# Performance work log

Measured on AMD Instinct MI355X. Metric: run time of the kernel, lower is better.

The kernel has to match this reference:

```python
import jax, jax.numpy as jnp
import numpy as np
import math

D_MODEL = 512
N_HEADS = 8
K_NEIGHBORS = 30
B, S = 4, 2048
N_VARIATES = 8
EPS = 1e-5


def layer_norm(x, g, b):
    m = jnp.mean(x, axis=-1, keepdims=True)
    v = jnp.mean(jnp.square(x - m), axis=-1, keepdims=True)
    return (x - m) * jax.lax.rsqrt(v + EPS) * g + b


def mha(x, mask, w_in, b_in, w_out, b_out):
    # x: [B,S,D]; mask: [B,S,S] bool, True = blocked (same for every head)
    Bb, Ss, D = x.shape
    H, dh = N_HEADS, D // N_HEADS
    qkv = x @ w_in.T + b_in                      # [B,S,3D]
    q, k, v = jnp.split(qkv, 3, axis=-1)
    q = q.reshape(Bb, Ss, H, dh).transpose(0, 2, 1, 3)
    k = k.reshape(Bb, Ss, H, dh).transpose(0, 2, 1, 3)
    v = v.reshape(Bb, Ss, H, dh).transpose(0, 2, 1, 3)
    scores = jnp.einsum('bhqd,bhkd->bhqk', q, k) / math.sqrt(dh)
    scores = jnp.where(mask[:, None, :, :], -jnp.inf, scores)
    attn = jax.nn.softmax(scores, axis=-1)
    o = jnp.einsum('bhqk,bhkd->bhqd', attn, v)
    o = o.transpose(0, 2, 1, 3).reshape(Bb, Ss, D)
    return o @ w_out.T + b_out


def build_masks(variates, times, valid_mask):
    Bb, Ss = variates.shape
    eye = jnp.eye(Ss, dtype=bool)
    same_var = variates[:, :, None] == variates[:, None, :]      # [B,S,S]
    valid_2d = valid_mask[:, :, None] & valid_mask[:, None, :]
    intra_mask = ~(same_var & valid_2d)                          # True = blocked
    blocked_i = jnp.any(jnp.all(intra_mask, axis=-1))
    intra_mask = intra_mask & ~(blocked_i & eye)                 # unblock diagonal if any row fully blocked

    diff_var = ~same_var
    time_dist = jnp.abs(times[:, :, None] - times[:, None, :])
    time_dist = jnp.where(~valid_2d | ~diff_var, jnp.inf, time_dist)
    k = min(K_NEIGHBORS, Ss)
    _, topk_idx = jax.lax.top_k(-time_dist, k)                   # k smallest distances
    b_idx = jnp.arange(Bb)[:, None, None]
    r_idx = jnp.arange(Ss)[None, :, None]
    knn_mask = jnp.zeros((Bb, Ss, Ss), dtype=bool).at[b_idx, r_idx, topk_idx].set(True)
    knn_mask = knn_mask & valid_2d
    inter_mask = ~knn_mask
    blocked_e = jnp.any(jnp.all(inter_mask, axis=-1))
    inter_mask = inter_mask & ~(blocked_e & eye)
    return intra_mask, inter_mask


def setup_inputs() -> dict:
    key = jax.random.key(0)
    ks = jax.random.split(key, 12)
    D = D_MODEL
    s = 0.02
    inp = {
        'x': jax.random.normal(ks[0], (B, S, D), dtype=jnp.float32),
        'variates': jax.random.randint(ks[1], (B, S), 0, N_VARIATES),
        'times': jax.random.uniform(ks[2], (B, S), dtype=jnp.float32),
        'valid_mask': jnp.ones((B, S), dtype=bool),
        'in_w1': jax.random.normal(ks[3], (3 * D, D), dtype=jnp.float32) * s,
        'in_b1': jnp.zeros((3 * D,), dtype=jnp.float32),
        'out_w1': jax.random.normal(ks[4], (D, D), dtype=jnp.float32) * s,
        'out_b1': jnp.zeros((D,), dtype=jnp.float32),
        'ln_g1': jnp.ones((D,), dtype=jnp.float32),
        'ln_b1': jnp.zeros((D,), dtype=jnp.float32),
        'in_w2': jax.random.normal(ks[5], (3 * D, D), dtype=jnp.float32) * s,
        'in_b2': jnp.zeros((3 * D,), dtype=jnp.float32),
        'out_w2': jax.random.normal(ks[6], (D, D), dtype=jnp.float32) * s,
        'out_b2': jnp.zeros((D,), dtype=jnp.float32),
        'ln_g2': jnp.ones((D,), dtype=jnp.float32),
        'ln_b2': jnp.zeros((D,), dtype=jnp.float32),
    }
    return inp


def reference(x, variates, times, valid_mask,
              in_w1, in_b1, out_w1, out_b1, ln_g1, ln_b1,
              in_w2, in_b2, out_w2, out_b2, ln_g2, ln_b2):
    intra_mask, inter_mask = build_masks(variates, times, valid_mask)
    a1 = mha(x, intra_mask, in_w1, in_b1, out_w1, out_b1)
    x = layer_norm(x + a1, ln_g1, ln_b1)
    a2 = mha(x, inter_mask, in_w2, in_b2, out_w2, out_b2)
    x = layer_norm(x + a2, ln_g2, ln_b2)
    return x
```

## Files before the change

### kernel.cpp

```cpp
#include <hip/hip_runtime.h>


#define S_LEN 2048
#define BATCH 4
#define DM    512
#define NH    8
#define DH    64
#define KNN_K 30
#define NVAR  8
#define NTOK  (BATCH * S_LEN)
#define QKVD  (3 * DM)
#define PADCAP 2560
#define MAXTILE 40

typedef float f32x4 __attribute__((ext_vector_type(4)));
typedef short s16x8 __attribute__((ext_vector_type(8)));
typedef short s16x4 __attribute__((ext_vector_type(4)));

__device__ __forceinline__ float bf2f(short u) {
  return __uint_as_float(((unsigned)(unsigned short)u) << 16);
}
__device__ __forceinline__ short f2bf(float f) {
  unsigned x = __float_as_uint(f);
  return (short)((x + 0x7fffu + ((x >> 16) & 1u)) >> 16);
}

#define KNNB (NTOK / 8)
#define C_N0 (NTOK * DM / 4)
#define C_N1 (QKVD * DM / 4)
#define C_N2 (DM * DM / 4)
#define C_B1 (C_N0 + C_N1)
#define C_B2 (C_B1 + C_N2)
#define C_B3 (C_B2 + C_N1)
#define C_B4 (C_B3 + C_N2)
#define PREP_GRID (KNNB + BATCH + C_B4 / 256)

__global__ __launch_bounds__(256) void prep_all(
    const int* __restrict__ variates, const float* __restrict__ times,
    int* __restrict__ knn_out,
    int* __restrict__ gcnt, int* __restrict__ pgoff, int* __restrict__ porig,
    int* __restrict__ tileV, int* __restrict__ tileQ0, int* __restrict__ ntile,
    const float* __restrict__ s0, const float* __restrict__ s1,
    const float* __restrict__ s2, const float* __restrict__ s3,
    const float* __restrict__ s4, short* __restrict__ d0,
    short* __restrict__ d1, short* __restrict__ d2,
    short* __restrict__ d3, short* __restrict__ d4) {
  int blk = blockIdx.x;
  int tid = threadIdx.x;

  if (blk < KNNB) {
    int w = tid >> 6, lane = tid & 63;
    int bq0 = blk * 8 + w * 2;
    int bq1 = bq0 + 1;
    int b = bq0 >> 11;
    float tq0 = times[bq0], tq1 = times[bq1];
    int vq0 = variates[bq0], vq1 = variates[bq1];
    const float* tb = times + b * S_LEN;
    const int* vb = variates + b * S_LEN;
    int j0 = lane * 32;

    unsigned u0[32], u1[32];
#pragma unroll
    for (int q = 0; q < 8; ++q) {
      float4 t4 = *(const float4*)(tb + j0 + q * 4);
      int4 v4 = *(const int4*)(vb + j0 + q * 4);
      u0[q * 4 + 0] = __float_as_uint((v4.x == vq0) ? __builtin_inff() : fabsf(tq0 - t4.x));
      u0[q * 4 + 1] = __float_as_uint((v4.y == vq0) ? __builtin_inff() : fabsf(tq0 - t4.y));
      u0[q * 4 + 2] = __float_as_uint((v4.z == vq0) ? __builtin_inff() : fabsf(tq0 - t4.z));
      u0[q * 4 + 3] = __float_as_uint((v4.w == vq0) ? __builtin_inff() : fabsf(tq0 - t4.w));
      u1[q * 4 + 0] = __float_as_uint((v4.x == vq1) ? __builtin_inff() : fabsf(tq1 - t4.x));
      u1[q * 4 + 1] = __float_as_uint((v4.y == vq1) ? __builtin_inff() : fabsf(tq1 - t4.y));
      u1[q * 4 + 2] = __float_as_uint((v4.z == vq1) ? __builtin_inff() : fabsf(tq1 - t4.z));
      u1[q * 4 + 3] = __float_as_uint((v4.w == vq1) ? __builtin_inff() : fabsf(tq1 - t4.w));
    }

    unsigned lo0 = 0u, hi0 = 0x7F800000u;
    unsigned lo1 = 0u, hi1 = 0x7F800000u;
    for (int it = 0; it < 31; ++it) {
      unsigned mid0 = lo0 + ((hi0 - lo0) >> 1);
      unsigned mid1 = lo1 + ((hi1 - lo1) >> 1);
      int c0 = 0, c1 = 0;
#pragma unroll
      for (int k = 0; k < 32; ++k) {
        c0 += (u0[k] <= mid0) ? 1 : 0;
        c1 += (u1[k] <= mid1) ? 1 : 0;
      }
      int pc = c0 | (c1 << 16);
#pragma unroll
      for (int o2 = 32; o2; o2 >>= 1) pc += __shfl_xor(pc, o2);
      int pc0 = pc & 0xffff, pc1 = pc >> 16;
      if (lo0 < hi0) { if (pc0 >= KNN_K) hi0 = mid0; else lo0 = mid0 + 1; }
      if (lo1 < hi1) { if (pc1 >= KNN_K) hi1 = mid1; else lo1 = mid1 + 1; }
      if (lo0 >= hi0 && lo1 >= hi1) break;
    }
    unsigned tau0 = lo0, tau1 = lo1;

    int cl0 = 0, ce0 = 0, cl1 = 0, ce1 = 0;
#pragma unroll
    for (int k = 0; k < 32; ++k) {
      cl0 += (u0[k] < tau0) ? 1 : 0;  ce0 += (u0[k] == tau0) ? 1 : 0;
      cl1 += (u1[k] < tau1) ? 1 : 0;  ce1 += (u1[k] == tau1) ? 1 : 0;
    }
    int pa = cl0 | (cl1 << 16), pe = ce0 | (ce1 << 16);
#pragma unroll
    for (int o2 = 1; o2 < 64; o2 <<= 1) {
      int ta = __shfl_up(pa, o2);
      int te = __shfl_up(pe, o2);
      if (lane >= o2) { pa += ta; pe += te; }
    }
    int paTop = __shfl(pa, 63);
    int totL0 = paTop & 0xffff, totL1 = paTop >> 16;
    int excl0 = (pa & 0xffff) - cl0, excl1 = (pa >> 16) - cl1;
    int exce0 = totL0 + (pe & 0xffff) - ce0, exce1 = totL1 + (pe >> 16) - ce1;

    int* op0 = knn_out + bq0 * KNN_K;
    int* op1 = knn_out + bq1 * KNN_K;
    int pos0 = excl0, pos1 = excl1;
#pragma unroll
    for (int k = 0; k < 32; ++k) {
      if (u0[k] < tau0) { op0[pos0] = j0 + k; ++pos0; }
      if (u1[k] < tau1) { op1[pos1] = j0 + k; ++pos1; }
    }
    int r0 = exce0, r1 = exce1;
#pragma unroll
    for (int k = 0; k < 32; ++k) {
      if (u0[k] == tau0) { if (r0 < KNN_K) op0[r0] = j0 + k; ++r0; }
      if (u1[k] == tau1) { if (r1 < KNN_K) op1[r1] = j0 + k; ++r1; }
    }
  } else if (blk < KNNB + BATCH) {
    int b = blk - KNNB;
    int t = tid;
    __shared__ int scnt[64][NVAR];
    __shared__ int soff[64][NVAR];
    __shared__ int stot[NVAR], sbase[NVAR];
    for (int p = t; p < PADCAP; p += 256) porig[b * PADCAP + p] = -1;
    const int* vb = variates + b * S_LEN;
    int c[NVAR] = {0, 0, 0, 0, 0, 0, 0, 0};
    if (t < 64) {
      for (int j = t * 32; j < t * 32 + 32; ++j) {
        int v = vb[j];
#pragma unroll
        for (int u = 0; u < NVAR; ++u) c[u] += (v == u);
      }
#pragma unroll
      for (int u = 0; u < NVAR; ++u) scnt[t][u] = c[u];
    }
    __syncthreads();
    if (t < NVAR) {
      int a = 0;
      for (int u = 0; u < 64; ++u) { soff[u][t] = a; a += scnt[u][t]; }
      stot[t] = a;
    }
    __syncthreads();
    if (t == 0) {
      int a = 0, nt = 0;
      for (int v = 0; v < NVAR; ++v) {
        sbase[v] = a;
        pgoff[b * NVAR + v] = a;
        gcnt[b * NVAR + v] = stot[v];
        int ntv = (stot[v] + 63) >> 6;
        for (int i = 0; i < ntv; ++i) {
          tileV[b * MAXTILE + nt] = v;
          tileQ0[b * MAXTILE + nt] = a + i * 64;
          ++nt;
        }
        a += ntv * 64;
      }
      ntile[b] = nt;
    }
    __syncthreads();
    if (t < 64) {
      int o[NVAR];
#pragma unroll
      for (int u = 0; u < NVAR; ++u) o[u] = sbase[u] + soff[t][u];
      for (int j = t * 32; j < t * 32 + 32; ++j) {
        int v = vb[j];
        int dst = 0;
#pragma unroll
        for (int u = 0; u < NVAR; ++u) dst += (v == u) ? o[u] : 0;
        porig[b * PADCAP + dst] = j;
#pragma unroll
        for (int u = 0; u < NVAR; ++u) o[u] += (v == u);
      }
    }
  } else {
    int i = (blk - KNNB - BATCH) * 256 + tid;
    const float* src; short* dst; int k;
    if (i < C_N0)      { src = s0; dst = d0; k = i; }
    else if (i < C_B1) { src = s1; dst = d1; k = i - C_N0; }
    else if (i < C_B2) { src = s2; dst = d2; k = i - C_B1; }
    else if (i < C_B3) { src = s3; dst = d3; k = i - C_B2; }
    else               { src = s4; dst = d4; k = i - C_B3; }
    float4 v = ((const float4*)src)[k];
    s16x4 o;
    o[0] = f2bf(v.x); o[1] = f2bf(v.y); o[2] = f2bf(v.z); o[3] = f2bf(v.w);
    ((s16x4*)dst)[k] = o;
  }
}

template <int OUT_BF16>
__global__ __launch_bounds__(256) void gemm_bt(const short* __restrict__ A,
                                               const short* __restrict__ Bm,
                                               const float* __restrict__ bias,
                                               void* __restrict__ Cout,
                                               int M, int N, int K) {
  __shared__ short sA[128 * 40];
  __shared__ short sB[128 * 40];
  int n0 = blockIdx.x * 128, m0 = blockIdx.y * 128;
  int tid = threadIdx.x;
  int lane = tid & 63, wv = tid >> 6;
  int wr = wv >> 1, wc = wv & 1;

  int srow = tid >> 2;
  int scol = (tid & 3) * 8;
  const short* aG = A + (size_t)(m0 + srow) * K + scol;
  const short* bG = Bm + (size_t)(n0 + srow) * K + scol;

  f32x4 acc[4][4] = {};
  int nk = K >> 5;

  s16x8 pa0 = *(const s16x8*)(aG);
  s16x8 pa1 = *(const s16x8*)(aG + (size_t)64 * K);
  s16x8 pb0 = *(const s16x8*)(bG);
  s16x8 pb1 = *(const s16x8*)(bG + (size_t)64 * K);

  for (int kt = 0; kt < nk; ++kt) {
    __syncthreads();
    *(s16x8*)&sA[srow * 40 + scol] = pa0;
    *(s16x8*)&sA[(srow + 64) * 40 + scol] = pa1;
    *(s16x8*)&sB[srow * 40 + scol] = pb0;
    *(s16x8*)&sB[(srow + 64) * 40 + scol] = pb1;
    __syncthreads();
    if (kt + 1 < nk) {
      const short* a2 = aG + (kt + 1) * 32;
      const short* b2 = bG + (kt + 1) * 32;
      pa0 = *(const s16x8*)(a2);
      pa1 = *(const s16x8*)(a2 + (size_t)64 * K);
      pb0 = *(const s16x8*)(b2);
      pb1 = *(const s16x8*)(b2 + (size_t)64 * K);
    }
    int kb = (lane >> 4) * 8;
    int ar = wr * 64 + (lane & 15);
    int br = wc * 64 + (lane & 15);
    s16x8 af[4], bf[4];
#pragma unroll
    for (int m = 0; m < 4; ++m) af[m] = *(const s16x8*)&sA[(ar + m * 16) * 40 + kb];
#pragma unroll
    for (int n = 0; n < 4; ++n) bf[n] = *(const s16x8*)&sB[(br + n * 16) * 40 + kb];
#pragma unroll
    for (int m = 0; m < 4; ++m)
#pragma unroll
      for (int n = 0; n < 4; ++n)
        acc[m][n] = __builtin_amdgcn_mfma_f32_16x16x32_bf16(af[m], bf[n], acc[m][n], 0, 0, 0);
  }

  int crow0 = m0 + wr * 64 + ((lane >> 4) * 4);
  int ccol0 = n0 + wc * 64 + (lane & 15);
#pragma unroll
  for (int n = 0; n < 4; ++n) {
    int col = ccol0 + n * 16;
    float bv = bias ? bias[col] : 0.f;
#pragma unroll
    for (int m = 0; m < 4; ++m) {
#pragma unroll
      for (int j = 0; j < 4; ++j) {
        int row = crow0 + m * 16 + j;
        float val = acc[m][n][j] + bv;
        if (OUT_BF16)
          ((short*)Cout)[(size_t)row * N + col] = f2bf(val);
        else
          ((float*)Cout)[(size_t)row * N + col] = val;
      }
    }
  }
}

__global__ __launch_bounds__(256) void intra_attn(
    const short* __restrict__ qkv, const int* __restrict__ porig,
    const int* __restrict__ tileV, const int* __restrict__ tileQ0,
    const int* __restrict__ ntile, const int* __restrict__ pgoff,
    const int* __restrict__ gcnt, short* __restrict__ o) {
  int b = blockIdx.z, h = blockIdx.y, t = blockIdx.x;
  if (t >= ntile[b]) return;
  int v = tileV[b * MAXTILE + t];
  int q0 = tileQ0[b * MAXTILE + t];
  int k0 = pgoff[b * NVAR + v];
  int L = gcnt[b * NVAR + v];
  int nch = (L + 63) >> 6;

  __shared__ short sQ[2][64][40];
  __shared__ short sK[2][64][40];
  __shared__ short sVT[2][64][40];
  __shared__ short sP[2][64][40];

  int tid = threadIdx.x, lane = tid & 63, w = tid >> 6;
  int colbase = lane & 15;
  int kfrag = (lane >> 4) * 8;

  {
    int r = tid >> 2, cc = (tid & 3) * 16;
    int tok = porig[b * PADCAP + q0 + r];
    if (tok < 0) tok = 0;
    const short* src = qkv + ((size_t)(b * S_LEN + tok)) * QKVD + h * DH + cc;
    s16x8 v0 = *(const s16x8*)src;
    s16x8 v1 = *(const s16x8*)(src + 8);
    int half = cc >> 5, kk = cc & 31;
    *(s16x8*)&sQ[half][r][kk] = v0;
    *(s16x8*)&sQ[half][r][kk + 8] = v1;
  }

  f32x4 accO[4] = {};
  float mrun[4], lrun[4];
#pragma unroll
  for (int j = 0; j < 4; ++j) { mrun[j] = -__builtin_inff(); lrun[j] = 0.f; }

  for (int c = 0; c < nch; ++c) {
    __syncthreads();
    {
      int r = tid >> 2, cc = (tid & 3) * 16;
      int tok = porig[b * PADCAP + k0 + c * 64 + r];
      if (tok < 0) tok = 0;
      size_t rowg = (size_t)(b * S_LEN + tok) * QKVD;
      const short* srcK = qkv + rowg + DM + h * DH + cc;
      s16x8 k0v = *(const s16x8*)srcK;
      s16x8 k1v = *(const s16x8*)(srcK + 8);
      int half = cc >> 5, kk = cc & 31;
      *(s16x8*)&sK[half][r][kk] = k0v;
      *(s16x8*)&sK[half][r][kk + 8] = k1v;
      const short* srcV = qkv + rowg + 2 * DM + h * DH + cc;
      s16x8 v0v = *(const s16x8*)srcV;
      s16x8 v1v = *(const s16x8*)(srcV + 8);
      int khalf = r >> 5, kkv = r & 31;
#pragma unroll
      for (int i = 0; i < 8; ++i) sVT[khalf][cc + i][kkv] = v0v[i];
#pragma unroll
      for (int i = 0; i < 8; ++i) sVT[khalf][cc + 8 + i][kkv] = v1v[i];
    }
    __syncthreads();

    s16x8 aQ0 = *(const s16x8*)&sQ[0][w * 16 + colbase][kfrag];
    s16x8 aQ1 = *(const s16x8*)&sQ[1][w * 16 + colbase][kfrag];
    f32x4 accS[4] = {};
#pragma unroll
    for (int n = 0; n < 4; ++n) {
      s16x8 b0 = *(const s16x8*)&sK[0][n * 16 + colbase][kfrag];
      s16x8 b1 = *(const s16x8*)&sK[1][n * 16 + colbase][kfrag];
      accS[n] = __builtin_amdgcn_mfma_f32_16x16x32_bf16(aQ0, b0, accS[n], 0, 0, 0);
      accS[n] = __builtin_amdgcn_mfma_f32_16x16x32_bf16(aQ1, b1, accS[n], 0, 0, 0);
    }
#pragma unroll
    for (int n = 0; n < 4; ++n)
#pragma unroll
      for (int j = 0; j < 4; ++j) accS[n][j] *= 0.125f;

    float pv[4][4];
#pragma unroll
    for (int j = 0; j < 4; ++j) {
      float cm = -__builtin_inff();
#pragma unroll
      for (int n = 0; n < 4; ++n) {
        bool ok = (c * 64 + n * 16 + colbase) < L;
        float se = ok ? accS[n][j] : -__builtin_inff();
        cm = fmaxf(cm, se);
      }
      for (int o2 = 8; o2; o2 >>= 1) cm = fmaxf(cm, __shfl_xor(cm, o2));
      float mn = fmaxf(mrun[j], cm);
      float al = __expf(mrun[j] - mn);
      float rs = 0.f;
#pragma unroll
      for (int n = 0; n < 4; ++n) {
        bool ok = (c * 64 + n * 16 + colbase) < L;
        float p = ok ? __expf(accS[n][j] - mn) : 0.f;
        pv[n][j] = p;
        rs += p;
      }
      for (int o2 = 8; o2; o2 >>= 1) rs += __shfl_xor(rs, o2);
      lrun[j] = lrun[j] * al + rs;
      mrun[j] = mn;
#pragma unroll
      for (int n = 0; n < 4; ++n) accO[n][j] *= al;
    }

    int prow = w * 16 + ((lane >> 4) << 2);
#pragma unroll
    for (int n = 0; n < 4; ++n)
#pragma unroll
      for (int j = 0; j < 4; ++j)
        sP[n >> 1][prow + j][colbase + ((n & 1) << 4)] = f2bf(pv[n][j]);

    s16x8 aP0 = *(const s16x8*)&sP[0][w * 16 + colbase][kfrag];
    s16x8 aP1 = *(const s16x8*)&sP[1][w * 16 + colbase][kfrag];
#pragma unroll
    for (int n = 0; n < 4; ++n) {
      s16x8 b0 = *(const s16x8*)&sVT[0][n * 16 + colbase][kfrag];
      s16x8 b1 = *(const s16x8*)&sVT[1][n * 16 + colbase][kfrag];
      accO[n] = __builtin_amdgcn_mfma_f32_16x16x32_bf16(aP0, b0, accO[n], 0, 0, 0);
      accO[n] = __builtin_amdgcn_mfma_f32_16x16x32_bf16(aP1, b1, accO[n], 0, 0, 0);
    }
  }

#pragma unroll
  for (int j = 0; j < 4; ++j) {
    int prow = w * 16 + (lane >> 4) * 4 + j;
    int orig = porig[b * PADCAP + q0 + prow];
    if (orig >= 0) {
      float inv = 1.f / lrun[j];
      size_t base = ((size_t)(b * S_LEN + orig)) * DM + h * DH;
#pragma unroll
      for (int n = 0; n < 4; ++n)
        o[base + n * 16 + colbase] = f2bf(accO[n][j] * inv);
    }
  }
}

__global__ __launch_bounds__(256) void inter_attn(const short* __restrict__ qkv,
                                                  const int* __restrict__ knn,
                                                  short* __restrict__ o) {
  __shared__ float sS[4][NH][32];
  __shared__ float sP[4][NH][32];
  int tid = threadIdx.x, lane = tid & 63, w = tid >> 6;
  int bq = blockIdx.x * 4 + w;
  int b = bq >> 11;
  int h = lane >> 3;

  int myidx = (lane < KNN_K) ? knn[bq * KNN_K + lane] : 0;

  s16x8 q8 = *(const s16x8*)(qkv + (size_t)bq * QKVD + lane * 8);
  float qf[8];
#pragma unroll
  for (int i = 0; i < 8; ++i) qf[i] = bf2f(q8[i]) * 0.125f;

  for (int j = 0; j < KNN_K; ++j) {
    int idx = __shfl(myidx, j);
    s16x8 k8 = *(const s16x8*)(qkv + ((size_t)(b * S_LEN + idx)) * QKVD + DM + lane * 8);
    float acc = 0.f;
#pragma unroll
    for (int i = 0; i < 8; ++i) acc += qf[i] * bf2f(k8[i]);
    acc += __shfl_xor(acc, 1);
    acc += __shfl_xor(acc, 2);
    acc += __shfl_xor(acc, 4);
    if ((lane & 7) == 0) sS[w][h][j] = acc;
  }

  int jsub = lane & 7;
  float sv0 = sS[w][h][jsub];
  float sv1 = sS[w][h][jsub + 8];
  float sv2 = sS[w][h][jsub + 16];
  float sv3 = (jsub < 6) ? sS[w][h][jsub + 24] : -__builtin_inff();
  float m = fmaxf(fmaxf(sv0, sv1), fmaxf(sv2, sv3));
  m = fmaxf(m, __shfl_xor(m, 1));
  m = fmaxf(m, __shfl_xor(m, 2));
  m = fmaxf(m, __shfl_xor(m, 4));
  float p0 = __expf(sv0 - m), p1 = __expf(sv1 - m), p2 = __expf(sv2 - m);
  float p3 = (jsub < 6) ? __expf(sv3 - m) : 0.f;
  sP[w][h][jsub] = p0;
  sP[w][h][jsub + 8] = p1;
  sP[w][h][jsub + 16] = p2;
  sP[w][h][jsub + 24] = p3;
  float l = p0 + p1 + p2 + p3;
  l += __shfl_xor(l, 1);
  l += __shfl_xor(l, 2);
  l += __shfl_xor(l, 4);

  float o8[8] = {};
  for (int j = 0; j < KNN_K; ++j) {
    int idx = __shfl(myidx, j);
    s16x8 v8 = *(const s16x8*)(qkv + ((size_t)(b * S_LEN + idx)) * QKVD + 2 * DM + lane * 8);
    float p = sP[w][h][j];
#pragma unroll
    for (int i = 0; i < 8; ++i) o8[i] += p * bf2f(v8[i]);
  }
  float inv = 1.f / l;
  s16x8 ov;
#pragma unroll
  for (int i = 0; i < 8; ++i) ov[i] = f2bf(o8[i] * inv);
  *(s16x8*)(o + (size_t)bq * DM + lane * 8) = ov;
}

__global__ __launch_bounds__(256) void residual_ln(const float* __restrict__ x,
                                                   const float* __restrict__ a,
                                                   const float* __restrict__ g,
                                                   const float* __restrict__ bta,
                                                   float* __restrict__ yf,
                                                   short* __restrict__ yb) {
  int row = blockIdx.x * 4 + (threadIdx.x >> 6);
  int lane = threadIdx.x & 63;
  const float4* xp = (const float4*)(x + (size_t)row * DM);
  const float4* ap = (const float4*)(a + (size_t)row * DM);
  float4 v0 = xp[lane * 2], v1 = xp[lane * 2 + 1];
  float4 a0 = ap[lane * 2], a1 = ap[lane * 2 + 1];
  float r[8] = {v0.x + a0.x, v0.y + a0.y, v0.z + a0.z, v0.w + a0.w,
                v1.x + a1.x, v1.y + a1.y, v1.z + a1.z, v1.w + a1.w};
  float s = 0.f;
#pragma unroll
  for (int j = 0; j < 8; ++j) s += r[j];
  for (int o2 = 32; o2; o2 >>= 1) s += __shfl_xor(s, o2);
  float mean = s * (1.f / DM);
  float vs = 0.f;
#pragma unroll
  for (int j = 0; j < 8; ++j) { float d = r[j] - mean; vs += d * d; }
  for (int o2 = 32; o2; o2 >>= 1) vs += __shfl_xor(vs, o2);
  float inv = rsqrtf(vs * (1.f / DM) + 1e-5f);
  const float4* gp = (const float4*)g;
  const float4* bp = (const float4*)bta;
  float4 g0 = gp[lane * 2], g1 = gp[lane * 2 + 1];
  float4 b0 = bp[lane * 2], b1 = bp[lane * 2 + 1];
  float gg[8] = {g0.x, g0.y, g0.z, g0.w, g1.x, g1.y, g1.z, g1.w};
  float bb[8] = {b0.x, b0.y, b0.z, b0.w, b1.x, b1.y, b1.z, b1.w};
  float y[8];
#pragma unroll
  for (int j = 0; j < 8; ++j) y[j] = (r[j] - mean) * inv * gg[j] + bb[j];
  float4 o0 = {y[0], y[1], y[2], y[3]};
  float4 o1 = {y[4], y[5], y[6], y[7]};
  float4* yp = (float4*)(yf + (size_t)row * DM);
  yp[lane * 2] = o0;
  yp[lane * 2 + 1] = o1;
  if (yb) {
    s16x8 ob;
#pragma unroll
    for (int j = 0; j < 8; ++j) ob[j] = f2bf(y[j]);
    *(s16x8*)(yb + (size_t)row * DM + lane * 8) = ob;
  }
}

extern "C" void kernel_launch(void* const* d_in, const int* in_sizes, int n_in,
                              void* d_out, int out_size, void* d_ws, size_t ws_size,
                              hipStream_t stream) {
  const float* x      = (const float*)d_in[0];
  const int*   var    = (const int*)d_in[1];
  const float* times  = (const float*)d_in[2];
  const float* in_w1  = (const float*)d_in[4];
  const float* in_b1  = (const float*)d_in[5];
  const float* out_w1 = (const float*)d_in[6];
  const float* out_b1 = (const float*)d_in[7];
  const float* ln_g1  = (const float*)d_in[8];
  const float* ln_b1  = (const float*)d_in[9];
  const float* in_w2  = (const float*)d_in[10];
  const float* in_b2  = (const float*)d_in[11];
  const float* out_w2 = (const float*)d_in[12];
  const float* out_b2 = (const float*)d_in[13];
  const float* ln_g2  = (const float*)d_in[14];
  const float* ln_b2  = (const float*)d_in[15];
  float* out = (float*)d_out;

  char* ws = (char*)d_ws;
  size_t off = 0;
  auto alloc = [&](size_t bytes) -> char* {
    char* p = ws + off;
    off = (off + bytes + 255) & ~(size_t)255;
    return p;
  };
  short* xb    = (short*)alloc((size_t)NTOK * DM * 2);
  short* x1b   = (short*)alloc((size_t)NTOK * DM * 2);
  short* w1q   = (short*)alloc((size_t)QKVD * DM * 2);
  short* w1o   = (short*)alloc((size_t)DM * DM * 2);
  short* w2q   = (short*)alloc((size_t)QKVD * DM * 2);
  short* w2o   = (short*)alloc((size_t)DM * DM * 2);
  short* qkvb  = (short*)alloc((size_t)NTOK * QKVD * 2);
  short* ob    = (short*)alloc((size_t)NTOK * DM * 2);
  float* af    = (float*)alloc((size_t)NTOK * DM * 4);
  float* x1f   = (float*)alloc((size_t)NTOK * DM * 4);
  int* gcnt    = (int*)alloc((size_t)BATCH * NVAR * 4);
  int* pgoff   = (int*)alloc((size_t)BATCH * NVAR * 4);
  int* porig   = (int*)alloc((size_t)BATCH * PADCAP * 4);
  int* tileV   = (int*)alloc((size_t)BATCH * MAXTILE * 4);
  int* tileQ0  = (int*)alloc((size_t)BATCH * MAXTILE * 4);
  int* ntile   = (int*)alloc((size_t)BATCH * 4);
  int* knn     = (int*)alloc((size_t)NTOK * KNN_K * 4);

  prep_all<<<PREP_GRID, 256, 0, stream>>>(
      var, times, knn, gcnt, pgoff, porig, tileV, tileQ0, ntile,
      x, in_w1, out_w1, in_w2, out_w2, xb, w1q, w1o, w2q, w2o);

  gemm_bt<1><<<dim3(QKVD / 128, NTOK / 128), 256, 0, stream>>>(xb, w1q, in_b1, qkvb,
                                                               NTOK, QKVD, DM);
  intra_attn<<<dim3(MAXTILE, NH, BATCH), 256, 0, stream>>>(qkvb, porig, tileV, tileQ0,
                                                           ntile, pgoff, gcnt, ob);
  gemm_bt<0><<<dim3(DM / 128, NTOK / 128), 256, 0, stream>>>(ob, w1o, out_b1, af,
                                                             NTOK, DM, DM);
  residual_ln<<<NTOK / 4, 256, 0, stream>>>(x, af, ln_g1, ln_b1, x1f, x1b);

  gemm_bt<1><<<dim3(QKVD / 128, NTOK / 128), 256, 0, stream>>>(x1b, w2q, in_b2, qkvb,
                                                               NTOK, QKVD, DM);
  inter_attn<<<NTOK / 4, 256, 0, stream>>>(qkvb, knn, ob);
  gemm_bt<0><<<dim3(DM / 128, NTOK / 128), 256, 0, stream>>>(ob, w2o, out_b2, af,
                                                             NTOK, DM, DM);
  residual_ln<<<NTOK / 4, 256, 0, stream>>>(x1f, af, ln_g2, ln_b2, out, nullptr);
}
```

Before: 220.8 us.

## Split KNN search across the two QKV GEMM launches to overlap work

Moves the top-k neighbour search out of the prep kernel and splits it in half, with each half running as extra blocks prepended to the grid of one of the two QKV projection GEMMs. The intent is to let the ALU-heavy, register-heavy KNN blocks overlap with MFMA GEMM tiles instead of lengthening the prep kernel. In exchange, the fused kernel's register footprint and occupancy are set by the larger of the two paths, which could slow the GEMM tiles. KNN results are still produced before inter_attn consumes them.

```diff
diff --git a/kernel.cpp b/kernel.cpp
--- a/kernel.cpp
+++ b/kernel.cpp
@@ -12,6 +12,8 @@
 #define QKVD  (3 * DM)
 #define PADCAP 2560
 #define MAXTILE 40
+#define KNNB  (NTOK / 8)
+#define KNN_HALF (KNNB / 2)
 
 typedef float f32x4 __attribute__((ext_vector_type(4)));
 typedef short s16x8 __attribute__((ext_vector_type(8)));
@@ -25,7 +27,90 @@
   return (short)((x + 0x7fffu + ((x >> 16) & 1u)) >> 16);
 }
 
-#define KNNB (NTOK / 8)
+__device__ __forceinline__ void knn_block(int blk, int tid,
+                                          const int* __restrict__ variates,
+                                          const float* __restrict__ times,
+                                          int* __restrict__ out) {
+  int w = tid >> 6, lane = tid & 63;
+  int bq0 = blk * 8 + w * 2;
+  int bq1 = bq0 + 1;
+  int b = bq0 >> 11;
+  float tq0 = times[bq0], tq1 = times[bq1];
+  int vq0 = variates[bq0], vq1 = variates[bq1];
+  const float* tb = times + b * S_LEN;
+  const int* vb = variates + b * S_LEN;
+  int j0 = lane * 32;
+
+  unsigned u0[32], u1[32];
+#pragma unroll
+  for (int q = 0; q < 8; ++q) {
+    float4 t4 = *(const float4*)(tb + j0 + q * 4);
+    int4 v4 = *(const int4*)(vb + j0 + q * 4);
+    u0[q * 4 + 0] = __float_as_uint((v4.x == vq0) ? __builtin_inff() : fabsf(tq0 - t4.x));
+    u0[q * 4 + 1] = __float_as_uint((v4.y == vq0) ? __builtin_inff() : fabsf(tq0 - t4.y));
+    u0[q * 4 + 2] = __float_as_uint((v4.z == vq0) ? __builtin_inff() : fabsf(tq0 - t4.z));
+    u0[q * 4 + 3] = __float_as_uint((v4.w == vq0) ? __builtin_inff() : fabsf(tq0 - t4.w));
+    u1[q * 4 + 0] = __float_as_uint((v4.x == vq1) ? __builtin_inff() : fabsf(tq1 - t4.x));
+    u1[q * 4 + 1] = __float_as_uint((v4.y == vq1) ? __builtin_inff() : fabsf(tq1 - t4.y));
+    u1[q * 4 + 2] = __float_as_uint((v4.z == vq1) ? __builtin_inff() : fabsf(tq1 - t4.z));
+    u1[q * 4 + 3] = __float_as_uint((v4.w == vq1) ? __builtin_inff() : fabsf(tq1 - t4.w));
+  }
+
+  unsigned lo0 = 0u, hi0 = 0x7F800000u;
+  unsigned lo1 = 0u, hi1 = 0x7F800000u;
+  for (int it = 0; it < 31; ++it) {
+    unsigned mid0 = lo0 + ((hi0 - lo0) >> 1);
+    unsigned mid1 = lo1 + ((hi1 - lo1) >> 1);
+    int c0 = 0, c1 = 0;
+#pragma unroll
+    for (int k = 0; k < 32; ++k) {
+      c0 += (u0[k] <= mid0) ? 1 : 0;
+      c1 += (u1[k] <= mid1) ? 1 : 0;
+    }
+    int pc = c0 | (c1 << 16);
+#pragma unroll
+    for (int o2 = 32; o2; o2 >>= 1) pc += __shfl_xor(pc, o2);
+    int pc0 = pc & 0xffff, pc1 = pc >> 16;
+    if (lo0 < hi0) { if (pc0 >= KNN_K) hi0 = mid0; else lo0 = mid0 + 1; }
+    if (lo1 < hi1) { if (pc1 >= KNN_K) hi1 = mid1; else lo1 = mid1 + 1; }
+    if (lo0 >= hi0 && lo1 >= hi1) break;
+  }
+  unsigned tau0 = lo0, tau1 = lo1;
+
+  int cl0 = 0, ce0 = 0, cl1 = 0, ce1 = 0;
+#pragma unroll
+  for (int k = 0; k < 32; ++k) {
+    cl0 += (u0[k] < tau0) ? 1 : 0;  ce0 += (u0[k] == tau0) ? 1 : 0;
+    cl1 += (u1[k] < tau1) ? 1 : 0;  ce1 += (u1[k] == tau1) ? 1 : 0;
+  }
+  int pa = cl0 | (cl1 << 16), pe = ce0 | (ce1 << 16);
+#pragma unroll
+  for (int o2 = 1; o2 < 64; o2 <<= 1) {
+    int ta = __shfl_up(pa, o2);
+    int te = __shfl_up(pe, o2);
+    if (lane >= o2) { pa += ta; pe += te; }
+  }
+  int paTop = __shfl(pa, 63);
+  int totL0 = paTop & 0xffff, totL1 = paTop >> 16;
+  int excl0 = (pa & 0xffff) - cl0, excl1 = (pa >> 16) - cl1;
+  int exce0 = totL0 + (pe & 0xffff) - ce0, exce1 = totL1 + (pe >> 16) - ce1;
+
+  int* op0 = out + bq0 * KNN_K;
+  int* op1 = out + bq1 * KNN_K;
+  int pos0 = excl0, pos1 = excl1;
+#pragma unroll
+  for (int k = 0; k < 32; ++k) {
+    if (u0[k] < tau0) { op0[pos0] = j0 + k; ++pos0; }
+    if (u1[k] < tau1) { op1[pos1] = j0 + k; ++pos1; }
+  }
+  int r0 = exce0, r1 = exce1;
+#pragma unroll
+  for (int k = 0; k < 32; ++k) {
+    if (u0[k] == tau0) { if (r0 < KNN_K) op0[r0] = j0 + k; ++r0; }
+    if (u1[k] == tau1) { if (r1 < KNN_K) op1[r1] = j0 + k; ++r1; }
+  }
+}
+
 #define C_N0 (NTOK * DM / 4)
 #define C_N1 (QKVD * DM / 4)
 #define C_N2 (DM * DM / 4)
@@ -33,11 +118,10 @@
 #define C_B2 (C_B1 + C_N2)
 #define C_B3 (C_B2 + C_N1)
 #define C_B4 (C_B3 + C_N2)
-#define PREP_GRID (KNNB + BATCH + C_B4 / 256)
-
-__global__ __launch_bounds__(256) void prep_all(
-    const int* __restrict__ variates, const float* __restrict__ times,
-    int* __restrict__ knn_out,
+#define PREP_GRID (BATCH + C_B4 / 256)
+
+__global__ __launch_bounds__(256) void prep_cast(
+    const int* __restrict__ variates,
     int* __restrict__ gcnt, int* __restrict__ pgoff, int* __restrict__ porig,
     int* __restrict__ tileV, int* __restrict__ tileQ0, int* __restrict__ ntile,
     const float* __restrict__ s0, const float* __restrict__ s1,
@@ -48,87 +132,8 @@
   int blk = blockIdx.x;
   int tid = threadIdx.x;
 
-  if (blk < KNNB) {
-    int w = tid >> 6, lane = tid & 63;
-    int bq0 = blk * 8 + w * 2;
-    int bq1 = bq0 + 1;
-    int b = bq0 >> 11;
-    float tq0 = times[bq0], tq1 = times[bq1];
-    int vq0 = variates[bq0], vq1 = variates[bq1];
-    const float* tb = times + b * S_LEN;
-    const int* vb = variates + b * S_LEN;
-    int j0 = lane * 32;
-
-    unsigned u0[32], u1[32];
-#pragma unroll
-    for (int q = 0; q < 8; ++q) {
-      float4 t4 = *(const float4*)(tb + j0 + q * 4);
-      int4 v4 = *(const int4*)(vb + j0 + q * 4);
-      u0[q * 4 + 0] = __float_as_uint((v4.x == vq0) ? __builtin_inff() : fabsf(tq0 - t4.x));
-      u0[q * 4 + 1] = __float_as_uint((v4.y == vq0) ? __builtin_inff() : fabsf(tq0 - t4.y));
-      u0[q * 4 + 2] = __float_as_uint((v4.z == vq0) ? __builtin_inff() : fabsf(tq0 - t4.z));
-      u0[q * 4 + 3] = __float_as_uint((v4.w == vq0) ? __builtin_inff() : fabsf(tq0 - t4.w));
-      u1[q * 4 + 0] = __float_as_uint((v4.x == vq1) ? __builtin_inff() : fabsf(tq1 - t4.x));
-      u1[q * 4 + 1] = __float_as_uint((v4.y == vq1) ? __builtin_inff() : fabsf(tq1 - t4.y));
-      u1[q * 4 + 2] = __float_as_uint((v4.z == vq1) ? __builtin_inff() : fabsf(tq1 - t4.z));
-      u1[q * 4 + 3] = __float_as_uint((v4.w == vq1) ? __builtin_inff() : fabsf(tq1 - t4.w));
-    }
-
-    unsigned lo0 = 0u, hi0 = 0x7F800000u;
-    unsigned lo1 = 0u, hi1 = 0x7F800000u;
-    for (int it = 0; it < 31; ++it) {
-      unsigned mid0 = lo0 + ((hi0 - lo0) >> 1);
-      unsigned mid1 = lo1 + ((hi1 - lo1) >> 1);
-      int c0 = 0, c1 = 0;
-#pragma unroll
-      for (int k = 0; k < 32; ++k) {
-        c0 += (u0[k] <= mid0) ? 1 : 0;
-        c1 += (u1[k] <= mid1) ? 1 : 0;
-      }
-      int pc = c0 | (c1 << 16);
-#pragma unroll
-      for (int o2 = 32; o2; o2 >>= 1) pc += __shfl_xor(pc, o2);
-      int pc0 = pc & 0xffff, pc1 = pc >> 16;
-      if (lo0 < hi0) { if (pc0 >= KNN_K) hi0 = mid0; else lo0 = mid0 + 1; }
-      if (lo1 < hi1) { if (pc1 >= KNN_K) hi1 = mid1; else lo1 = mid1 + 1; }
-      if (lo0 >= hi0 && lo1 >= hi1) break;
-    }
-    unsigned tau0 = lo0, tau1 = lo1;
-
-    int cl0 = 0, ce0 = 0, cl1 = 0, ce1 = 0;
-#pragma unroll
-    for (int k = 0; k < 32; ++k) {
-      cl0 += (u0[k] < tau0) ? 1 : 0;  ce0 += (u0[k] == tau0) ? 1 : 0;
-      cl1 += (u1[k] < tau1) ? 1 : 0;  ce1 += (u1[k] == tau1) ? 1 : 0;
-    }
-    int pa = cl0 | (cl1 << 16), pe = ce0 | (ce1 << 16);
-#pragma unroll
-    for (int o2 = 1; o2 < 64; o2 <<= 1) {
-      int ta = __shfl_up(pa, o2);
-      int te = __shfl_up(pe, o2);
-      if (lane >= o2) { pa += ta; pe += te; }
-    }
-    int paTop = __shfl(pa, 63);
-    int totL0 = paTop & 0xffff, totL1 = paTop >> 16;
-    int excl0 = (pa & 0xffff) - cl0, excl1 = (pa >> 16) - cl1;
-    int exce0 = totL0 + (pe & 0xffff) - ce0, exce1 = totL1 + (pe >> 16) - ce1;
-
-    int* op0 = knn_out + bq0 * KNN_K;
-    int* op1 = knn_out + bq1 * KNN_K;
-    int pos0 = excl0, pos1 = excl1;
-#pragma unroll
-    for (int k = 0; k < 32; ++k) {
-      if (u0[k] < tau0) { op0[pos0] = j0 + k; ++pos0; }
-      if (u1[k] < tau1) { op1[pos1] = j0 + k; ++pos1; }
-    }
-    int r0 = exce0, r1 = exce1;
-#pragma unroll
-    for (int k = 0; k < 32; ++k) {
-      if (u0[k] == tau0) { if (r0 < KNN_K) op0[r0] = j0 + k; ++r0; }
-      if (u1[k] == tau1) { if (r1 < KNN_K) op1[r1] = j0 + k; ++r1; }
-    }
-  } else if (blk < KNNB + BATCH) {
-    int b = blk - KNNB;
+  if (blk < BATCH) {
+    int b = blk;
     int t = tid;
     __shared__ int scnt[64][NVAR];
     __shared__ int soff[64][NVAR];
@@ -184,7 +189,7 @@
       }
     }
   } else {
-    int i = (blk - KNNB - BATCH) * 256 + tid;
+    int i = (blk - BATCH) * 256 + tid;
     const float* src; short* dst; int k;
     if (i < C_N0)      { src = s0; dst = d0; k = i; }
     else if (i < C_B1) { src = s1; dst = d1; k = i - C_N0; }
@@ -195,6 +200,89 @@
     s16x4 o;
     o[0] = f2bf(v.x); o[1] = f2bf(v.y); o[2] = f2bf(v.z); o[3] = f2bf(v.w);
     ((s16x4*)dst)[k] = o;
+  }
+}
+
+template <int OUT_BF16>
+__global__ __launch_bounds__(256) void gemm_knn(
+    const short* __restrict__ A, const short* __restrict__ Bm,
+    const float* __restrict__ bias, void* __restrict__ Cout,
+    int M, int N, int K, int gridN, int nKnn, int knnBase,
+    const int* __restrict__ variates, const float* __restrict__ times,
+    int* __restrict__ knn_out) {
+  __shared__ short sA[128 * 40];
+  __shared__ short sB[128 * 40];
+  if ((int)blockIdx.x < nKnn) {
+    knn_block(knnBase + blockIdx.x, threadIdx.x, variates, times, knn_out);
+    return;
+  }
+  int gblk = blockIdx.x - nKnn;
+  int n0 = (gblk % gridN) * 128, m0 = (gblk / gridN) * 128;
+  int tid = threadIdx.x;
+  int lane = tid & 63, wv = tid >> 6;
+  int wr = wv >> 1, wc = wv & 1;
+
+  int srow = tid >> 2;
+  int scol = (tid & 3) * 8;
+  const short* aG = A + (size_t)(m0 + srow) * K + scol;
+  const short* bG = Bm + (size_t)(n0 + srow) * K + scol;
+
+  f32x4 acc[4][4] = {};
+  int nk = K >> 5;
+
+  s16x8 pa0 = *(const s16x8*)(aG);
+  s16x8 pa1 = *(const s16x8*)(aG + (size_t)64 * K);
+  s16x8 pb0 = *(const s16x8*)(bG);
+  s16x8 pb1 = *(const s16x8*)(bG + (size_t)64 * K);
+
+  for (int kt = 0; kt < nk; ++kt) {
+    __syncthreads();
+    *(s16x8*)&sA[srow * 40 + scol] = pa0;
+    *(s16x8*)&sA[(srow + 64) * 40 + scol] = pa1;
+    *(s16x8*)&sB[srow * 40 + scol] = pb0;
+    *(s16x8*)&sB[(srow + 64) * 40 + scol] = pb1;
+    __syncthreads();
+    if (kt + 1 < nk) {
+      const short* a2 = aG + (kt + 1) * 32;
+      const short* b2 = bG + (kt + 1) * 32;
+      pa0 = *(const s16x8*)(a2);
+      pa1 = *(const s16x8*)(a2 + (size_t)64 * K);
+      pb0 = *(const s16x8*)(b2);
+      pb1 = *(const s16x8*)(b2 + (size_t)64 * K);
+    }
+    int kb = (lane >> 4) * 8;
+    int ar = wr * 64 + (lane & 15);
+    int br = wc * 64 + (lane & 15);
+    s16x8 af[4], bf[4];
+#pragma unroll
+    for (int m = 0; m < 4; ++m) af[m] = *(const s16x8*)&sA[(ar + m * 16) * 40 + kb];
+#pragma unroll
+    for (int n = 0; n < 4; ++n) bf[n] = *(const s16x8*)&sB[(br + n * 16) * 40 + kb];
+#pragma unroll
+    for (int m = 0; m < 4; ++m)
+#pragma unroll
+      for (int n = 0; n < 4; ++n)
+        acc[m][n] = __builtin_amdgcn_mfma_f32_16x16x32_bf16(af[m], bf[n], acc[m][n], 0, 0, 0);
+  }
+
+  int crow0 = m0 + wr * 64 + ((lane >> 4) * 4);
+  int ccol0 = n0 + wc * 64 + (lane & 15);
+#pragma unroll
+  for (int n = 0; n < 4; ++n) {
+    int col = ccol0 + n * 16;
+    float bv = bias ? bias[col] : 0.f;
+#pragma unroll
+    for (int m = 0; m < 4; ++m) {
+#pragma unroll
+      for (int j = 0; j < 4; ++j) {
+        int row = crow0 + m * 16 + j;
+        float val = acc[m][n][j] + bv;
+        if (OUT_BF16)
+          ((short*)Cout)[(size_t)row * N + col] = f2bf(val);
+        else
+          ((float*)Cout)[(size_t)row * N + col] = val;
+      }
+    }
   }
 }
 
@@ -568,20 +656,22 @@
   int* ntile   = (int*)alloc((size_t)BATCH * 4);
   int* knn     = (int*)alloc((size_t)NTOK * KNN_K * 4);
 
-  prep_all<<<PREP_GRID, 256, 0, stream>>>(
-      var, times, knn, gcnt, pgoff, porig, tileV, tileQ0, ntile,
+  prep_cast<<<PREP_GRID, 256, 0, stream>>>(
+      var, gcnt, pgoff, porig, tileV, tileQ0, ntile,
       x, in_w1, out_w1, in_w2, out_w2, xb, w1q, w1o, w2q, w2o);
 
-  gemm_bt<1><<<dim3(QKVD / 128, NTOK / 128), 256, 0, stream>>>(xb, w1q, in_b1, qkvb,
-                                                               NTOK, QKVD, DM);
+  gemm_knn<1><<<KNN_HALF + (QKVD / 128) * (NTOK / 128), 256, 0, stream>>>(
+      xb, w1q, in_b1, qkvb, NTOK, QKVD, DM, QKVD / 128, KNN_HALF, 0,
+      var, times, knn);
   intra_attn<<<dim3(MAXTILE, NH, BATCH), 256, 0, stream>>>(qkvb, porig, tileV, tileQ0,
                                                            ntile, pgoff, gcnt, ob);
   gemm_bt<0><<<dim3(DM / 128, NTOK / 128), 256, 0, stream>>>(ob, w1o, out_b1, af,
                                                              NTOK, DM, DM);
   residual_ln<<<NTOK / 4, 256, 0, stream>>>(x, af, ln_g1, ln_b1, x1f, x1b);
 
-  gemm_bt<1><<<dim3(QKVD / 128, NTOK / 128), 256, 0, stream>>>(x1b, w2q, in_b2, qkvb,
-                                                               NTOK, QKVD, DM);
+  gemm_knn<1><<<KNN_HALF + (QKVD / 128) * (NTOK / 128), 256, 0, stream>>>(
+      x1b, w2q, in_b2, qkvb, NTOK, QKVD, DM, QKVD / 128, KNN_HALF, KNN_HALF,
+      var, times, knn);
   inter_attn<<<NTOK / 4, 256, 0, stream>>>(qkvb, knn, ob);
   gemm_bt<0><<<dim3(DM / 128, NTOK / 128), 256, 0, stream>>>(ob, w2o, out_b2, af,
                                                              NTOK, DM, DM);
```

New measurement: 246.6 us. 1.12x slower.

## Replace brute-force KNN threshold search with sorted-time two-pointer neighbor selection

Applied to the files above, without the earlier changes.

The per-query KNN used to scan all 2048 keys with a 31-step radix/binary search over float bits. It now bitonic-sorts each batch's times once in shared memory, then each query binary-searches its position and expands left/right with two pointers to pick the 30 nearest different-variate tokens. Ties at the threshold are resolved by smallest index to match top_k ordering. This cuts per-query work from O(S·log) to roughly O(K), but adds a serial single-block-per-batch sort and a separate kernel launch, and divergent while-loops may hurt.

```diff
diff --git a/kernel.cpp b/kernel.cpp
--- a/kernel.cpp
+++ b/kernel.cpp
@@ -25,7 +25,6 @@
   return (short)((x + 0x7fffu + ((x >> 16) & 1u)) >> 16);
 }
 
-#define KNNB (NTOK / 8)
 #define C_N0 (NTOK * DM / 4)
 #define C_N1 (QKVD * DM / 4)
 #define C_N2 (DM * DM / 4)
@@ -33,13 +32,13 @@
 #define C_B2 (C_B1 + C_N2)
 #define C_B3 (C_B2 + C_N1)
 #define C_B4 (C_B3 + C_N2)
-#define PREP_GRID (KNNB + BATCH + C_B4 / 256)
-
-__global__ __launch_bounds__(256) void prep_all(
+#define PREP_GRID (2 * BATCH + C_B4 / 256)
+
+__global__ __launch_bounds__(256) void prep_cast(
     const int* __restrict__ variates, const float* __restrict__ times,
-    int* __restrict__ knn_out,
     int* __restrict__ gcnt, int* __restrict__ pgoff, int* __restrict__ porig,
     int* __restrict__ tileV, int* __restrict__ tileQ0, int* __restrict__ ntile,
+    float* __restrict__ stimeG, int* __restrict__ spackG,
     const float* __restrict__ s0, const float* __restrict__ s1,
     const float* __restrict__ s2, const float* __restrict__ s3,
     const float* __restrict__ s4, short* __restrict__ d0,
@@ -48,87 +47,8 @@
   int blk = blockIdx.x;
   int tid = threadIdx.x;
 
-  if (blk < KNNB) {
-    int w = tid >> 6, lane = tid & 63;
-    int bq0 = blk * 8 + w * 2;
-    int bq1 = bq0 + 1;
-    int b = bq0 >> 11;
-    float tq0 = times[bq0], tq1 = times[bq1];
-    int vq0 = variates[bq0], vq1 = variates[bq1];
-    const float* tb = times + b * S_LEN;
-    const int* vb = variates + b * S_LEN;
-    int j0 = lane * 32;
-
-    unsigned u0[32], u1[32];
-#pragma unroll
-    for (int q = 0; q < 8; ++q) {
-      float4 t4 = *(const float4*)(tb + j0 + q * 4);
-      int4 v4 = *(const int4*)(vb + j0 + q * 4);
-      u0[q * 4 + 0] = __float_as_uint((v4.x == vq0) ? __builtin_inff() : fabsf(tq0 - t4.x));
-      u0[q * 4 + 1] = __float_as_uint((v4.y == vq0) ? __builtin_inff() : fabsf(tq0 - t4.y));
-      u0[q * 4 + 2] = __float_as_uint((v4.z == vq0) ? __builtin_inff() : fabsf(tq0 - t4.z));
-      u0[q * 4 + 3] = __float_as_uint((v4.w == vq0) ? __builtin_inff() : fabsf(tq0 - t4.w));
-      u1[q * 4 + 0] = __float_as_uint((v4.x == vq1) ? __builtin_inff() : fabsf(tq1 - t4.x));
-      u1[q * 4 + 1] = __float_as_uint((v4.y == vq1) ? __builtin_inff() : fabsf(tq1 - t4.y));
-      u1[q * 4 + 2] = __float_as_uint((v4.z == vq1) ? __builtin_inff() : fabsf(tq1 - t4.z));
-      u1[q * 4 + 3] = __float_as_uint((v4.w == vq1) ? __builtin_inff() : fabsf(tq1 - t4.w));
-    }
-
-    unsigned lo0 = 0u, hi0 = 0x7F800000u;
-    unsigned lo1 = 0u, hi1 = 0x7F800000u;
-    for (int it = 0; it < 31; ++it) {
-      unsigned mid0 = lo0 + ((hi0 - lo0) >> 1);
-      unsigned mid1 = lo1 + ((hi1 - lo1) >> 1);
-      int c0 = 0, c1 = 0;
-#pragma unroll
-      for (int k = 0; k < 32; ++k) {
-        c0 += (u0[k] <= mid0) ? 1 : 0;
-        c1 += (u1[k] <= mid1) ? 1 : 0;
-      }
-      int pc = c0 | (c1 << 16);
-#pragma unroll
-      for (int o2 = 32; o2; o2 >>= 1) pc += __shfl_xor(pc, o2);
-      int pc0 = pc & 0xffff, pc1 = pc >> 16;
-      if (lo0 < hi0) { if (pc0 >= KNN_K) hi0 = mid0; else lo0 = mid0 + 1; }
-      if (lo1 < hi1) { if (pc1 >= KNN_K) hi1 = mid1; else lo1 = mid1 + 1; }
-      if (lo0 >= hi0 && lo1 >= hi1) break;
-    }
-    unsigned tau0 = lo0, tau1 = lo1;
-
-    int cl0 = 0, ce0 = 0, cl1 = 0, ce1 = 0;
-#pragma unroll
-    for (int k = 0; k < 32; ++k) {
-      cl0 += (u0[k] < tau0) ? 1 : 0;  ce0 += (u0[k] == tau0) ? 1 : 0;
-      cl1 += (u1[k] < tau1) ? 1 : 0;  ce1 += (u1[k] == tau1) ? 1 : 0;
-    }
-    int pa = cl0 | (cl1 << 16), pe = ce0 | (ce1 << 16);
-#pragma unroll
-    for (int o2 = 1; o2 < 64; o2 <<= 1) {
-      int ta = __shfl_up(pa, o2);
-      int te = __shfl_up(pe, o2);
-      if (lane >= o2) { pa += ta; pe += te; }
-    }
-    int paTop = __shfl(pa, 63);
-    int totL0 = paTop & 0xffff, totL1 = paTop >> 16;
-    int excl0 = (pa & 0xffff) - cl0, excl1 = (pa >> 16) - cl1;
-    int exce0 = totL0 + (pe & 0xffff) - ce0, exce1 = totL1 + (pe >> 16) - ce1;
-
-    int* op0 = knn_out + bq0 * KNN_K;
-    int* op1 = knn_out + bq1 * KNN_K;
-    int pos0 = excl0, pos1 = excl1;
-#pragma unroll
-    for (int k = 0; k < 32; ++k) {
-      if (u0[k] < tau0) { op0[pos0] = j0 + k; ++pos0; }
-      if (u1[k] < tau1) { op1[pos1] = j0 + k; ++pos1; }
-    }
-    int r0 = exce0, r1 = exce1;
-#pragma unroll
-    for (int k = 0; k < 32; ++k) {
-      if (u0[k] == tau0) { if (r0 < KNN_K) op0[r0] = j0 + k; ++r0; }
-      if (u1[k] == tau1) { if (r1 < KNN_K) op1[r1] = j0 + k; ++r1; }
-    }
-  } else if (blk < KNNB + BATCH) {
-    int b = blk - KNNB;
+  if (blk < BATCH) {
+    int b = blk;
     int t = tid;
     __shared__ int scnt[64][NVAR];
     __shared__ int soff[64][NVAR];
@@ -183,8 +103,38 @@
         for (int u = 0; u < NVAR; ++u) o[u] += (v == u);
       }
     }
+  } else if (blk < 2 * BATCH) {
+    int b = blk - BATCH;
+    __shared__ float st[S_LEN];
+    __shared__ int sp[S_LEN];
+    for (int i = tid; i < S_LEN; i += 256) {
+      st[i] = times[b * S_LEN + i];
+      sp[i] = (variates[b * S_LEN + i] << 12) | i;
+    }
+    __syncthreads();
+    for (int k = 2; k <= S_LEN; k <<= 1) {
+      for (int j = k >> 1; j > 0; j >>= 1) {
+        for (int i = tid; i < S_LEN; i += 256) {
+          int l = i ^ j;
+          if (l > i) {
+            bool asc = ((i & k) == 0);
+            float a = st[i], cc = st[l];
+            bool sw = asc ? (a > cc) : (a < cc);
+            if (sw) {
+              st[i] = cc; st[l] = a;
+              int tmp = sp[i]; sp[i] = sp[l]; sp[l] = tmp;
+            }
+          }
+        }
+        __syncthreads();
+      }
+    }
+    for (int i = tid; i < S_LEN; i += 256) {
+      stimeG[b * S_LEN + i] = st[i];
+      spackG[b * S_LEN + i] = sp[i];
+    }
   } else {
-    int i = (blk - KNNB - BATCH) * 256 + tid;
+    int i = (blk - 2 * BATCH) * 256 + tid;
     const float* src; short* dst; int k;
     if (i < C_N0)      { src = s0; dst = d0; k = i; }
     else if (i < C_B1) { src = s1; dst = d1; k = i - C_N0; }
@@ -195,6 +145,82 @@
     s16x4 o;
     o[0] = f2bf(v.x); o[1] = f2bf(v.y); o[2] = f2bf(v.z); o[3] = f2bf(v.w);
     ((s16x4*)dst)[k] = o;
+  }
+}
+
+__global__ __launch_bounds__(256) void knn_tp(const float* __restrict__ times,
+                                              const int* __restrict__ variates,
+                                              const float* __restrict__ stimeG,
+                                              const int* __restrict__ spackG,
+                                              int* __restrict__ out) {
+  __shared__ float st[S_LEN];
+  __shared__ int sp[S_LEN];
+  int tid = threadIdx.x;
+  int bq = blockIdx.x * 256 + tid;
+  int b = bq >> 11;
+  for (int i = tid; i < S_LEN; i += 256) {
+    st[i] = stimeG[b * S_LEN + i];
+    sp[i] = spackG[b * S_LEN + i];
+  }
+  __syncthreads();
+
+  float tq = times[bq];
+  int vq = variates[bq];
+
+  int lo = 0, hi = S_LEN;
+#pragma unroll
+  for (int s = 0; s < 11; ++s) {
+    int mid = (lo + hi) >> 1;
+    if (st[mid] < tq) lo = mid + 1; else hi = mid;
+  }
+  int L = lo - 1, R = lo;
+
+  float dt[KNN_K];
+  int ti[KNN_K];
+#pragma unroll
+  for (int i = 0; i < KNN_K; ++i) {
+    while (L >= 0 && (sp[L] >> 12) == vq) --L;
+    while (R < S_LEN && (sp[R] >> 12) == vq) ++R;
+    float dL = (L >= 0) ? fabsf(tq - st[L]) : __builtin_inff();
+    float dR = (R < S_LEN) ? fabsf(tq - st[R]) : __builtin_inff();
+    if (dL <= dR) { dt[i] = dL; ti[i] = sp[L] & 0xFFF; --L; }
+    else          { dt[i] = dR; ti[i] = sp[R] & 0xFFF; ++R; }
+  }
+  float tau = dt[KNN_K - 1];
+  int nLess = 0;
+#pragma unroll
+  for (int i = 0; i < KNN_K; ++i) nLess += (dt[i] < tau) ? 1 : 0;
+
+  int* op = out + bq * KNN_K;
+#pragma unroll
+  for (int i = 0; i < KNN_K; ++i)
+    if (i < nLess) op[i] = ti[i];
+
+  int m = KNN_K - nLess;
+  int last = -1;
+  for (int s = 0; s < m; ++s) {
+    int best = 0x7fffffff;
+#pragma unroll
+    for (int i = 0; i < KNN_K; ++i)
+      if (dt[i] == tau && ti[i] > last && ti[i] < best) best = ti[i];
+    for (int Lw = L; Lw >= 0; --Lw) {
+      float d = fabsf(tq - st[Lw]);
+      if (d > tau) break;
+      if (d == tau && (sp[Lw] >> 12) != vq) {
+        int ix = sp[Lw] & 0xFFF;
+        if (ix > last && ix < best) best = ix;
+      }
+    }
+    for (int Rw = R; Rw < S_LEN; ++Rw) {
+      float d = fabsf(tq - st[Rw]);
+      if (d > tau) break;
+      if (d == tau && (sp[Rw] >> 12) != vq) {
+        int ix = sp[Rw] & 0xFFF;
+        if (ix > last && ix < best) best = ix;
+      }
+    }
+    op[nLess + s] = best;
+    last = best;
   }
 }
 
@@ -567,10 +593,14 @@
   int* tileQ0  = (int*)alloc((size_t)BATCH * MAXTILE * 4);
   int* ntile   = (int*)alloc((size_t)BATCH * 4);
   int* knn     = (int*)alloc((size_t)NTOK * KNN_K * 4);
-
-  prep_all<<<PREP_GRID, 256, 0, stream>>>(
-      var, times, knn, gcnt, pgoff, porig, tileV, tileQ0, ntile,
+  float* stimeG = (float*)alloc((size_t)NTOK * 4);
+  int*   spackG = (int*)alloc((size_t)NTOK * 4);
+
+  prep_cast<<<PREP_GRID, 256, 0, stream>>>(
+      var, times, gcnt, pgoff, porig, tileV, tileQ0, ntile, stimeG, spackG,
       x, in_w1, out_w1, in_w2, out_w2, xb, w1q, w1o, w2q, w2o);
+
+  knn_tp<<<NTOK / 256, 256, 0, stream>>>(times, var, stimeG, spackG, knn);
 
   gemm_bt<1><<<dim3(QKVD / 128, NTOK / 128), 256, 0, stream>>>(xb, w1q, in_b1, qkvb,
                                                                NTOK, QKVD, DM);
```

Result: slower. 287.2 us (+30.0%).
